# Optimization experiments

Hardware: AMD Instinct MI355X
Metric: run time of the kernel (lower is better)

Reference implementation:

```python
import jax, jax.numpy as jnp
import numpy as np
import math

T = 4096        # block_size / sequence length
E = 2048        # embedding_dim
D = 256         # head_dim


def setup_inputs() -> dict:
    key = jax.random.key(0)
    k_x, k_q, k_k, k_v = jax.random.split(key, 4)
    x = jax.random.normal(k_x, (T, E), dtype=jnp.float32)
    # nn.Linear weights are [out_features, in_features]
    s = 1.0 / math.sqrt(E)
    Wq = jax.random.normal(k_q, (D, E), dtype=jnp.float32) * s
    Wk = jax.random.normal(k_k, (D, E), dtype=jnp.float32) * s
    Wv = jax.random.normal(k_v, (D, E), dtype=jnp.float32) * s
    return {"x": x, "Wq": Wq, "Wk": Wk, "Wv": Wv}


def reference(x, Wq, Wk, Wv):
    # Projections: x @ W.T  (torch Linear, no bias)
    Q = x @ Wq.T            # [T, D]
    K = x @ Wk.T            # [T, D]
    V = x @ Wv.T            # [T, D]
    scale = 1.0 / math.sqrt(Q.shape[-1])
    scores = (Q @ K.T) * scale                      # [T, T]
    causal = jnp.tril(jnp.ones((T, T), dtype=bool))
    scores = jnp.where(causal, scores, jnp.float32(-1e10))
    probs = jax.nn.softmax(scores, axis=-1)         # row softmax (torch legacy dim=1 for 2-D)
    return probs @ V                                # [T, D]
```

## Files before the change

### kernel.cpp

```cpp
#include <hip/hip_runtime.h>
#include <hip/hip_bf16.h>

#define T_DIM 4096
#define E_DIM 2048
#define D_DIM 256

typedef __attribute__((ext_vector_type(4))) float f32x4;
typedef __attribute__((ext_vector_type(8))) short s16x8;

__device__ __forceinline__ unsigned short f2bf(float f) {
  unsigned int u = __float_as_uint(f);
  unsigned int r = (u + 0x7FFFu + ((u >> 16) & 1u)) >> 16;
  return (unsigned short)r;
}
__device__ __forceinline__ float bf2f(unsigned short h) {
  return __uint_as_float(((unsigned int)h) << 16);
}

__device__ __forceinline__ f32x4 mfma16(s16x8 a, s16x8 b, f32x4 c) {
  return __builtin_amdgcn_mfma_f32_16x16x32_bf16(a, b, c, 0, 0, 0);
}

__device__ __forceinline__ void gload_lds16(const void* g, void* l) {
  __builtin_amdgcn_global_load_lds((const __attribute__((address_space(1))) void*)g,
                                   (__attribute__((address_space(3))) void*)l, 16, 0, 0);
}

__device__ __forceinline__ int fbase(int t) {
  int g = t / 3, r = t - 3 * g;
  return 3 * g * (g + 1) / 2 + r * (g + 1);
}

__global__ __launch_bounds__(256) void cvt_kernel(const float* __restrict__ src,
                                                  unsigned short* __restrict__ dst, int n) {
  int i = blockIdx.x * blockDim.x + threadIdx.x;
  if (i * 8 + 8 <= n) {
    float4 a = ((const float4*)src)[i * 2];
    float4 b = ((const float4*)src)[i * 2 + 1];
    uint4 o;
    o.x = (unsigned int)f2bf(a.x) | ((unsigned int)f2bf(a.y) << 16);
    o.y = (unsigned int)f2bf(a.z) | ((unsigned int)f2bf(a.w) << 16);
    o.z = (unsigned int)f2bf(b.x) | ((unsigned int)f2bf(b.y) << 16);
    o.w = (unsigned int)f2bf(b.z) | ((unsigned int)f2bf(b.w) << 16);
    ((uint4*)dst)[i] = o;
  }
}

__global__ __launch_bounds__(256, 3) void qkv_gemm(
    const unsigned short* __restrict__ xb, const unsigned short* __restrict__ wb,
    unsigned short* __restrict__ Qg, unsigned short* __restrict__ Kg,
    unsigned short* __restrict__ Vt) {
  __shared__ __align__(16) unsigned short Al[2][128 * 64];
  __shared__ __align__(16) unsigned short Bl[2][64 * 64];
  int tid = threadIdx.x, wid = tid >> 6, lane = tid & 63;
  int lr = lane & 15, lk = lane >> 4;
  int bi_ = (int)blockIdx.x;
  int xcd = bi_ & 7, kk = bi_ >> 3;
  int mb_ = (kk / 12) * 8 + xcd, nb_ = kk % 12;
  int bm0 = mb_ * 128, bn0 = nb_ * 64;
  int wm = (wid >> 1) * 64, wn = (wid & 1) * 32;

  f32x4 acc[4][2];
#pragma unroll
  for (int m = 0; m < 4; ++m)
#pragma unroll
    for (int n = 0; n < 2; ++n) acc[m][n] = (f32x4){0.f, 0.f, 0.f, 0.f};

#define STAGE_QKV(kt, buf)                                                              \
  {                                                                                     \
    int k0 = (kt)*64;                                                                   \
    _Pragma("unroll") for (int i2 = 0; i2 < 4; ++i2) {                                  \
      int ci = (wid * 4 + i2) * 64 + lane;                                              \
      int row = ci >> 3, cc = ci & 7;                                                   \
      gload_lds16(&xb[(size_t)(bm0 + row) * E_DIM + k0 + ((cc ^ (row & 7)) << 3)],      \
                  &Al[buf][(size_t)(wid * 4 + i2) * 512]);                              \
    }                                                                                   \
    _Pragma("unroll") for (int i2 = 0; i2 < 2; ++i2) {                                  \
      int ci = (wid * 2 + i2) * 64 + lane;                                              \
      int row = ci >> 3, cc = ci & 7;                                                   \
      gload_lds16(&wb[(size_t)(bn0 + row) * E_DIM + k0 + ((cc ^ (row & 7)) << 3)],      \
                  &Bl[buf][(size_t)(wid * 2 + i2) * 512]);                              \
    }                                                                                   \
  }

  STAGE_QKV(0, 0);
  for (int kt = 0; kt < 32; ++kt) {
    int cur = kt & 1;
    __syncthreads();
    if (kt + 1 < 32) STAGE_QKV(kt + 1, cur ^ 1);
    s16x8 af[2][4], bfr[2][2];
#pragma unroll
    for (int c = 0; c < 2; ++c) {
#pragma unroll
      for (int m = 0; m < 4; ++m)
        af[c][m] = *(const s16x8*)&Al[cur][(size_t)(wm + m * 16 + lr) * 64 +
                                           (((c * 4 + lk) ^ (lr & 7)) << 3)];
#pragma unroll
      for (int n = 0; n < 2; ++n)
        bfr[c][n] = *(const s16x8*)&Bl[cur][(size_t)(wn + n * 16 + lr) * 64 +
                                            (((c * 4 + lk) ^ (lr & 7)) << 3)];
    }
#pragma unroll
    for (int c = 0; c < 2; ++c)
#pragma unroll
      for (int m = 0; m < 4; ++m)
#pragma unroll
        for (int n = 0; n < 2; ++n) acc[m][n] = mfma16(af[c][m], bfr[c][n], acc[m][n]);
  }

#pragma unroll
  for (int m = 0; m < 4; ++m) {
    int grow = bm0 + wm + m * 16 + lk * 4;
#pragma unroll
    for (int n = 0; n < 2; ++n) {
      int gcol = bn0 + wn + n * 16 + lr;
      unsigned short h[4];
#pragma unroll
      for (int r = 0; r < 4; ++r) h[r] = f2bf(acc[m][n][r]);
      if (gcol < 256) {
#pragma unroll
        for (int r = 0; r < 4; ++r) Qg[(size_t)(grow + r) * D_DIM + gcol] = h[r];
      } else if (gcol < 512) {
#pragma unroll
        for (int r = 0; r < 4; ++r) Kg[(size_t)(grow + r) * D_DIM + gcol - 256] = h[r];
      } else {
        uint2 w;
        w.x = (unsigned int)h[0] | ((unsigned int)h[1] << 16);
        w.y = (unsigned int)h[2] | ((unsigned int)h[3] << 16);
        *(uint2*)&Vt[(size_t)(gcol - 512) * T_DIM + grow] = w;
      }
    }
  }
#undef STAGE_QKV
}

__global__ __launch_bounds__(256, 2) void attn_kernel(
    const unsigned short* __restrict__ Qg, const unsigned short* __restrict__ Kg,
    const unsigned short* __restrict__ Vt, unsigned short* __restrict__ Opart,
    float* __restrict__ mpart, float* __restrict__ lpart) {
  __shared__ __align__(16) unsigned short Kl[2][32 * 256];
  __shared__ __align__(16) unsigned short Vl[2][256 * 32];
  __shared__ __align__(16) unsigned short Pl[4][16 * 40];

  int b = blockIdx.x;
  int t = (int)sqrtf(6.0f * (float)b + 2.25f);
  if (t > 63) t = 63;
  while (t > 0 && fbase(t) > b) --t;
  while (t < 63 && fbase(t + 1) <= b) ++t;
  int s = b - fbase(t);
  int nt = 2 * t + 2 - 6 * s;
  if (nt > 6) nt = 6;

  int tid = threadIdx.x, wid = tid >> 6, lane = tid & 63;
  int lr = lane & 15, lk = lane >> 4;
  int q0 = t * 64 + wid * 16;
  unsigned short* pl = &Pl[wid][0];

  s16x8 qf[8];
#pragma unroll
  for (int c = 0; c < 8; ++c)
    qf[c] = *(const s16x8*)&Qg[(size_t)(q0 + lr) * D_DIM + c * 32 + lk * 8];

  float m_run = -1e30f, l_run = 0.0f;
  f32x4 Oa[16];
#pragma unroll
  for (int d = 0; d < 16; ++d) Oa[d] = (f32x4){0.f, 0.f, 0.f, 0.f};
  const float scale = 0.0625f;

#define STAGE_KV(j, buf)                                                             \
  {                                                                                  \
    int kv_ = (j)*32;                                                                \
    _Pragma("unroll") for (int i2 = 0; i2 < 4; ++i2) {                               \
      int ci = (wid * 4 + i2) * 64 + lane;                                           \
      int row = ci >> 5, cc = ci & 31;                                               \
      gload_lds16(&Kg[(size_t)(kv_ + row) * D_DIM + ((cc ^ (row & 7)) << 3)],        \
                  &Kl[buf][(size_t)(wid * 4 + i2) * 512]);                           \
    }                                                                                \
    _Pragma("unroll") for (int i2 = 0; i2 < 4; ++i2) {                               \
      int ci = (wid * 4 + i2) * 64 + lane;                                           \
      int rr = ci >> 2, cc = ci & 3;                                                 \
      gload_lds16(&Vt[(size_t)rr * T_DIM + kv_ + ((cc ^ ((rr >> 1) & 3)) << 3)],     \
                  &Vl[buf][(size_t)(wid * 4 + i2) * 512]);                           \
    }                                                                                \
  }

  STAGE_KV(6 * s, 0);
  for (int n = 0; n < nt; ++n) {
    int j = 6 * s + n;
    int kv = j * 32;
    int cur = n & 1;
    __syncthreads();
    if (n + 1 < nt) STAGE_KV(j + 1, cur ^ 1);
    const unsigned short* kl = &Kl[cur][0];
    const unsigned short* vl = &Vl[cur][0];

    f32x4 sa[2];
    sa[0] = (f32x4){0.f, 0.f, 0.f, 0.f};
    sa[1] = (f32x4){0.f, 0.f, 0.f, 0.f};
#pragma unroll
    for (int jb = 0; jb < 2; ++jb) {
      int row = jb * 16 + lr;
#pragma unroll
      for (int c = 0; c < 8; ++c) {
        s16x8 kf = *(const s16x8*)&kl[(size_t)row * 256 + (((c * 4 + lk) ^ (lr & 7)) << 3)];
        sa[jb] = mfma16(kf, qf[c], sa[jb]);
      }
    }

    float tmax = -1e30f;
#pragma unroll
    for (int jb = 0; jb < 2; ++jb) {
#pragma unroll
      for (int r = 0; r < 4; ++r) {
        float v = sa[jb][r] * scale;
        int keyg = kv + jb * 16 + lk * 4 + r;
        if (keyg > q0 + lr) v = -1e30f;
        sa[jb][r] = v;
        tmax = fmaxf(tmax, v);
      }
    }
    tmax = fmaxf(tmax, __shfl_xor(tmax, 16));
    tmax = fmaxf(tmax, __shfl_xor(tmax, 32));
    float m_new = fmaxf(fmaxf(m_run, tmax), -1e29f);
    float alpha = __expf(m_run - m_new);
    float psum = 0.f;
#pragma unroll
    for (int jb = 0; jb < 2; ++jb) {
      float p0 = __expf(sa[jb][0] - m_new);
      float p1 = __expf(sa[jb][1] - m_new);
      float p2 = __expf(sa[jb][2] - m_new);
      float p3 = __expf(sa[jb][3] - m_new);
      psum += (p0 + p1) + (p2 + p3);
      uint2 w;
      w.x = (unsigned int)f2bf(p0) | ((unsigned int)f2bf(p1) << 16);
      w.y = (unsigned int)f2bf(p2) | ((unsigned int)f2bf(p3) << 16);
      *(uint2*)&pl[lr * 40 + jb * 16 + lk * 4] = w;
    }
    psum += __shfl_xor(psum, 16);
    psum += __shfl_xor(psum, 32);
    l_run = l_run * alpha + psum;
    m_run = m_new;
    float al[4];
#pragma unroll
    for (int r = 0; r < 4; ++r) al[r] = __shfl(alpha, lk * 4 + r);
#pragma unroll
    for (int d = 0; d < 16; ++d) {
#pragma unroll
      for (int r = 0; r < 4; ++r) Oa[d][r] *= al[r];
    }

    s16x8 pf = *(const s16x8*)&pl[lr * 40 + lk * 8];
    int vsw = (lk ^ ((lr >> 1) & 3)) << 3;
#pragma unroll
    for (int d = 0; d < 16; ++d) {
      s16x8 vf = *(const s16x8*)&vl[(size_t)(d * 16 + lr) * 32 + vsw];
      Oa[d] = mfma16(pf, vf, Oa[d]);
    }
  }

#pragma unroll
  for (int d = 0; d < 16; ++d) {
    unsigned short h[4];
#pragma unroll
    for (int r = 0; r < 4; ++r) h[r] = f2bf(Oa[d][r]);
    uint2 w;
    w.x = (unsigned int)h[0] | ((unsigned int)h[1] << 16);
    w.y = (unsigned int)h[2] | ((unsigned int)h[3] << 16);
    *(uint2*)&Opart[((size_t)b * 256 + d * 16 + lr) * 64 + wid * 16 + lk * 4] = w;
  }
  if (lane < 16) {
    mpart[(size_t)b * 64 + wid * 16 + lr] = m_run;
    lpart[(size_t)b * 64 + wid * 16 + lr] = l_run;
  }
#undef STAGE_KV
}

__global__ __launch_bounds__(256) void merge_kernel(const unsigned short* __restrict__ Opart,
                                                    const float* __restrict__ mpart,
                                                    const float* __restrict__ lpart,
                                                    float* __restrict__ out) {
  __shared__ float trans[64 * 65];
  int blk = blockIdx.x;
  int t = blk >> 2;
  int d0 = (blk & 3) * 64;
  int q0 = t * 64;
  int ql = threadIdx.x & 63;
  int dg = threadIdx.x >> 6;
  int g = t / 3, r3 = t - 3 * g;
  int base = 3 * g * (g + 1) / 2 + r3 * (g + 1);
  int nb = (t + 3) / 3;

  float M = -1e30f, den = 0.f;
  for (int p = 0; p < nb; ++p) {
    float mp = mpart[(size_t)(base + p) * 64 + ql];
    float lp = lpart[(size_t)(base + p) * 64 + ql];
    float Mn = fmaxf(M, mp);
    float sc = __expf(M - Mn);
    den = den * sc + __expf(mp - Mn) * lp;
    M = Mn;
  }
  float inv = 1.0f / den;

  float acc[16];
#pragma unroll
  for (int k = 0; k < 16; ++k) acc[k] = 0.f;
  for (int p = 0; p < nb; ++p) {
    float w = __expf(mpart[(size_t)(base + p) * 64 + ql] - M);
    const unsigned short* oprow = &Opart[((size_t)(base + p) * 256 + d0 + dg) * 64 + ql];
#pragma unroll
    for (int k = 0; k < 16; ++k) acc[k] += w * bf2f(oprow[(size_t)(4 * k) * 64]);
  }
#pragma unroll
  for (int k = 0; k < 16; ++k) trans[(dg + 4 * k) * 65 + ql] = acc[k] * inv;
  __syncthreads();

#pragma unroll
  for (int k = 0; k < 16; ++k) {
    int qq = (threadIdx.x >> 6) + 4 * k;
    int dd = threadIdx.x & 63;
    out[(size_t)(q0 + qq) * 256 + d0 + dd] = trans[dd * 65 + qq];
  }
}

extern "C" void kernel_launch(void* const* d_in, const int* in_sizes, int n_in,
                              void* d_out, int out_size, void* d_ws, size_t ws_size,
                              hipStream_t stream) {
  const float* x  = (const float*)d_in[0];
  const float* Wq = (const float*)d_in[1];
  const float* Wk = (const float*)d_in[2];
  const float* Wv = (const float*)d_in[3];

  char* ws = (char*)d_ws;
  unsigned short* xb = (unsigned short*)(ws);
  unsigned short* wb = (unsigned short*)(ws + 16777216);
  unsigned short* Qg = (unsigned short*)(ws + 19922944);
  unsigned short* Kg = (unsigned short*)(ws + 22020096);
  unsigned short* Vt = (unsigned short*)(ws + 24117248);
  unsigned short* Opart = (unsigned short*)(ws + 26214400);
  float* mpart = (float*)(ws + 49643520);
  float* lpart = (float*)(ws + 49826560);

  cvt_kernel<<<4096, 256, 0, stream>>>(x, xb, T_DIM * E_DIM);
  cvt_kernel<<<256, 256, 0, stream>>>(Wq, wb, D_DIM * E_DIM);
  cvt_kernel<<<256, 256, 0, stream>>>(Wk, wb + (size_t)D_DIM * E_DIM, D_DIM * E_DIM);
  cvt_kernel<<<256, 256, 0, stream>>>(Wv, wb + (size_t)2 * D_DIM * E_DIM, D_DIM * E_DIM);

  qkv_gemm<<<384, 256, 0, stream>>>(xb, wb, Qg, Kg, Vt);

  attn_kernel<<<715, 256, 0, stream>>>(Qg, Kg, Vt, Opart, mpart, lpart);

  merge_kernel<<<256, 256, 0, stream>>>(Opart, mpart, lpart, (float*)d_out);
}
```

Before: 108.4 us.

## Rework attention split into 128-query tiles, fuse conversions, single-pass merge

Merges the four fp32-to-bf16 conversion launches into one kernel. Replaces the qkv_gemm __syncthreads with raw barriers plus explicit vmcnt waits. Restructures attention to 512-thread blocks covering 128 queries, each handling a 128-key chunk as two 64-key tiles, with a new triangular block mapping interleaved across XCDs and causal masking skipped on off-diagonal tiles. The merge kernel now combines partials in a single online-rescaling pass over 128-query, 32-column tiles. The goal is fewer launches, fewer partials and better reuse per block, at the cost of larger LDS use and fewer, longer blocks.

```diff
diff --git a/kernel.cpp b/kernel.cpp
--- a/kernel.cpp
+++ b/kernel.cpp
@@ -26,24 +26,29 @@
                                    (__attribute__((address_space(3))) void*)l, 16, 0, 0);
 }
 
-__device__ __forceinline__ int fbase(int t) {
-  int g = t / 3, r = t - 3 * g;
-  return 3 * g * (g + 1) / 2 + r * (g + 1);
-}
-
-__global__ __launch_bounds__(256) void cvt_kernel(const float* __restrict__ src,
-                                                  unsigned short* __restrict__ dst, int n) {
-  int i = blockIdx.x * blockDim.x + threadIdx.x;
-  if (i * 8 + 8 <= n) {
-    float4 a = ((const float4*)src)[i * 2];
-    float4 b = ((const float4*)src)[i * 2 + 1];
-    uint4 o;
-    o.x = (unsigned int)f2bf(a.x) | ((unsigned int)f2bf(a.y) << 16);
-    o.y = (unsigned int)f2bf(a.z) | ((unsigned int)f2bf(a.w) << 16);
-    o.z = (unsigned int)f2bf(b.x) | ((unsigned int)f2bf(b.y) << 16);
-    o.w = (unsigned int)f2bf(b.z) | ((unsigned int)f2bf(b.w) << 16);
-    ((uint4*)dst)[i] = o;
-  }
+__global__ __launch_bounds__(256) void cvt_all(const float* __restrict__ x,
+                                               const float* __restrict__ wq,
+                                               const float* __restrict__ wk,
+                                               const float* __restrict__ wv,
+                                               unsigned short* __restrict__ xb,
+                                               unsigned short* __restrict__ wb) {
+  int blk = blockIdx.x;
+  const float* src;
+  unsigned short* dst;
+  int rel;
+  if (blk < 4096)      { src = x;  dst = xb;           rel = blk; }
+  else if (blk < 4352) { src = wq; dst = wb;           rel = blk - 4096; }
+  else if (blk < 4608) { src = wk; dst = wb + 524288;  rel = blk - 4352; }
+  else                 { src = wv; dst = wb + 1048576; rel = blk - 4608; }
+  int i = rel * 256 + threadIdx.x;
+  float4 a = ((const float4*)src)[i * 2];
+  float4 b = ((const float4*)src)[i * 2 + 1];
+  uint4 o;
+  o.x = (unsigned int)f2bf(a.x) | ((unsigned int)f2bf(a.y) << 16);
+  o.y = (unsigned int)f2bf(a.z) | ((unsigned int)f2bf(a.w) << 16);
+  o.z = (unsigned int)f2bf(b.x) | ((unsigned int)f2bf(b.y) << 16);
+  o.w = (unsigned int)f2bf(b.z) | ((unsigned int)f2bf(b.w) << 16);
+  ((uint4*)dst)[i] = o;
 }
 
 __global__ __launch_bounds__(256, 3) void qkv_gemm(
@@ -86,8 +91,14 @@
   STAGE_QKV(0, 0);
   for (int kt = 0; kt < 32; ++kt) {
     int cur = kt & 1;
-    __syncthreads();
-    if (kt + 1 < 32) STAGE_QKV(kt + 1, cur ^ 1);
+    __builtin_amdgcn_s_barrier();
+    if (kt + 1 < 32) {
+      STAGE_QKV(kt + 1, cur ^ 1);
+      asm volatile("s_waitcnt vmcnt(6)" ::: "memory");
+    } else {
+      asm volatile("s_waitcnt vmcnt(0)" ::: "memory");
+    }
+    __builtin_amdgcn_s_barrier();
     s16x8 af[2][4], bfr[2][2];
 #pragma unroll
     for (int c = 0; c < 2; ++c) {
@@ -134,87 +145,93 @@
 #undef STAGE_QKV
 }
 
-__global__ __launch_bounds__(256, 2) void attn_kernel(
+__global__ __launch_bounds__(512, 2) void attn_kernel(
     const unsigned short* __restrict__ Qg, const unsigned short* __restrict__ Kg,
     const unsigned short* __restrict__ Vt, unsigned short* __restrict__ Opart,
     float* __restrict__ mpart, float* __restrict__ lpart) {
-  __shared__ __align__(16) unsigned short Kl[2][32 * 256];
-  __shared__ __align__(16) unsigned short Vl[2][256 * 32];
-  __shared__ __align__(16) unsigned short Pl[4][16 * 40];
-
-  int b = blockIdx.x;
-  int t = (int)sqrtf(6.0f * (float)b + 2.25f);
-  if (t > 63) t = 63;
-  while (t > 0 && fbase(t) > b) --t;
-  while (t < 63 && fbase(t + 1) <= b) ++t;
-  int s = b - fbase(t);
-  int nt = 2 * t + 2 - 6 * s;
-  if (nt > 6) nt = 6;
+  __shared__ __align__(16) unsigned short Kl[2][64 * 256];
+  __shared__ __align__(16) unsigned short Vl[2][256 * 64];
+  __shared__ __align__(16) unsigned short Pl[8][16 * 64];
+
+  int bi = (int)blockIdx.x;
+  int j = (bi & 7) * 66 + (bi >> 3);
+  int t = (int)((sqrtf(8.0f * (float)j + 1.0f) - 1.0f) * 0.5f);
+  while (t > 0 && t * (t + 1) / 2 > j) --t;
+  while ((t + 1) * (t + 2) / 2 <= j) ++t;
+  int s = j - t * (t + 1) / 2;
 
   int tid = threadIdx.x, wid = tid >> 6, lane = tid & 63;
   int lr = lane & 15, lk = lane >> 4;
-  int q0 = t * 64 + wid * 16;
+  int q0w = t * 128 + wid * 16;
   unsigned short* pl = &Pl[wid][0];
 
-  s16x8 qf[8];
-#pragma unroll
-  for (int c = 0; c < 8; ++c)
-    qf[c] = *(const s16x8*)&Qg[(size_t)(q0 + lr) * D_DIM + c * 32 + lk * 8];
-
-  float m_run = -1e30f, l_run = 0.0f;
-  f32x4 Oa[16];
-#pragma unroll
-  for (int d = 0; d < 16; ++d) Oa[d] = (f32x4){0.f, 0.f, 0.f, 0.f};
-  const float scale = 0.0625f;
-
-#define STAGE_KV(j, buf)                                                             \
+#define STAGE_KV(jt, buf)                                                            \
   {                                                                                  \
-    int kv_ = (j)*32;                                                                \
+    int kv_ = (jt)*64;                                                               \
     _Pragma("unroll") for (int i2 = 0; i2 < 4; ++i2) {                               \
-      int ci = (wid * 4 + i2) * 64 + lane;                                           \
-      int row = ci >> 5, cc = ci & 31;                                               \
-      gload_lds16(&Kg[(size_t)(kv_ + row) * D_DIM + ((cc ^ (row & 7)) << 3)],        \
+      int idx = (wid * 4 + i2) * 64 + lane;                                          \
+      int row = idx >> 5, g = idx & 31;                                              \
+      gload_lds16(&Kg[(size_t)(kv_ + row) * D_DIM + ((g ^ (row & 7)) << 3)],         \
                   &Kl[buf][(size_t)(wid * 4 + i2) * 512]);                           \
     }                                                                                \
     _Pragma("unroll") for (int i2 = 0; i2 < 4; ++i2) {                               \
-      int ci = (wid * 4 + i2) * 64 + lane;                                           \
-      int rr = ci >> 2, cc = ci & 3;                                                 \
-      gload_lds16(&Vt[(size_t)rr * T_DIM + kv_ + ((cc ^ ((rr >> 1) & 3)) << 3)],     \
+      int idx = (wid * 4 + i2) * 64 + lane;                                          \
+      int d_ = idx >> 3, g = idx & 7;                                                \
+      gload_lds16(&Vt[(size_t)d_ * T_DIM + kv_ + ((g ^ (d_ & 7)) << 3)],             \
                   &Vl[buf][(size_t)(wid * 4 + i2) * 512]);                           \
     }                                                                                \
   }
 
-  STAGE_KV(6 * s, 0);
-  for (int n = 0; n < nt; ++n) {
-    int j = 6 * s + n;
-    int kv = j * 32;
-    int cur = n & 1;
-    __syncthreads();
-    if (n + 1 < nt) STAGE_KV(j + 1, cur ^ 1);
+  STAGE_KV(2 * s, 0);
+
+  s16x8 qf[8];
+#pragma unroll
+  for (int c = 0; c < 8; ++c)
+    qf[c] = *(const s16x8*)&Qg[(size_t)(q0w + lr) * D_DIM + c * 32 + lk * 8];
+
+  float m_run = -1e30f, l_run = 0.f;
+  f32x4 Oa[16];
+#pragma unroll
+  for (int d = 0; d < 16; ++d) Oa[d] = (f32x4){0.f, 0.f, 0.f, 0.f};
+  const float scale = 0.0625f;
+  int sw = lr & 7;
+
+#pragma unroll
+  for (int n = 0; n < 2; ++n) {
+    int jt = 2 * s + n, kv = jt * 64, cur = n;
+    __builtin_amdgcn_s_barrier();
+    if (n == 0) {
+      STAGE_KV(jt + 1, 1);
+      asm volatile("s_waitcnt vmcnt(8)" ::: "memory");
+    } else {
+      asm volatile("s_waitcnt vmcnt(0)" ::: "memory");
+    }
+    __builtin_amdgcn_s_barrier();
     const unsigned short* kl = &Kl[cur][0];
     const unsigned short* vl = &Vl[cur][0];
 
-    f32x4 sa[2];
-    sa[0] = (f32x4){0.f, 0.f, 0.f, 0.f};
-    sa[1] = (f32x4){0.f, 0.f, 0.f, 0.f};
-#pragma unroll
-    for (int jb = 0; jb < 2; ++jb) {
-      int row = jb * 16 + lr;
+    f32x4 sa[4];
+#pragma unroll
+    for (int jb = 0; jb < 4; ++jb) sa[jb] = (f32x4){0.f, 0.f, 0.f, 0.f};
+#pragma unroll
+    for (int jb = 0; jb < 4; ++jb) {
+      int rowbase = (jb * 16 + lr) * 256;
 #pragma unroll
       for (int c = 0; c < 8; ++c) {
-        s16x8 kf = *(const s16x8*)&kl[(size_t)row * 256 + (((c * 4 + lk) ^ (lr & 7)) << 3)];
+        s16x8 kf = *(const s16x8*)&kl[(size_t)rowbase + (((c * 4 + lk) ^ sw) << 3)];
         sa[jb] = mfma16(kf, qf[c], sa[jb]);
       }
     }
 
+    bool needmask = (kv + 63 > q0w);
+    int myq = q0w + lr;
     float tmax = -1e30f;
 #pragma unroll
-    for (int jb = 0; jb < 2; ++jb) {
+    for (int jb = 0; jb < 4; ++jb) {
 #pragma unroll
       for (int r = 0; r < 4; ++r) {
         float v = sa[jb][r] * scale;
-        int keyg = kv + jb * 16 + lk * 4 + r;
-        if (keyg > q0 + lr) v = -1e30f;
+        if (needmask && (kv + jb * 16 + lk * 4 + r) > myq) v = -1e30f;
         sa[jb][r] = v;
         tmax = fmaxf(tmax, v);
       }
@@ -225,7 +242,7 @@
     float alpha = __expf(m_run - m_new);
     float psum = 0.f;
 #pragma unroll
-    for (int jb = 0; jb < 2; ++jb) {
+    for (int jb = 0; jb < 4; ++jb) {
       float p0 = __expf(sa[jb][0] - m_new);
       float p1 = __expf(sa[jb][1] - m_new);
       float p2 = __expf(sa[jb][2] - m_new);
@@ -234,12 +251,13 @@
       uint2 w;
       w.x = (unsigned int)f2bf(p0) | ((unsigned int)f2bf(p1) << 16);
       w.y = (unsigned int)f2bf(p2) | ((unsigned int)f2bf(p3) << 16);
-      *(uint2*)&pl[lr * 40 + jb * 16 + lk * 4] = w;
+      *(uint2*)&pl[(size_t)lr * 64 + (((jb * 2 + (lk >> 1)) ^ sw) << 3) + (lk & 1) * 4] = w;
     }
     psum += __shfl_xor(psum, 16);
     psum += __shfl_xor(psum, 32);
     l_run = l_run * alpha + psum;
     m_run = m_new;
+
     float al[4];
 #pragma unroll
     for (int r = 0; r < 4; ++r) al[r] = __shfl(alpha, lk * 4 + r);
@@ -249,12 +267,18 @@
       for (int r = 0; r < 4; ++r) Oa[d][r] *= al[r];
     }
 
-    s16x8 pf = *(const s16x8*)&pl[lr * 40 + lk * 8];
-    int vsw = (lk ^ ((lr >> 1) & 3)) << 3;
+    s16x8 pf[2];
+#pragma unroll
+    for (int ks = 0; ks < 2; ++ks)
+      pf[ks] = *(const s16x8*)&pl[(size_t)lr * 64 + (((ks * 4 + lk) ^ sw) << 3)];
 #pragma unroll
     for (int d = 0; d < 16; ++d) {
-      s16x8 vf = *(const s16x8*)&vl[(size_t)(d * 16 + lr) * 32 + vsw];
-      Oa[d] = mfma16(pf, vf, Oa[d]);
+#pragma unroll
+      for (int ks = 0; ks < 2; ++ks) {
+        s16x8 vf = *(const s16x8*)&vl[(size_t)(d * 16 + lr) * 64 +
+                                      (((ks * 4 + lk) ^ sw) << 3)];
+        Oa[d] = mfma16(pf[ks], vf, Oa[d]);
+      }
     }
   }
 
@@ -266,11 +290,11 @@
     uint2 w;
     w.x = (unsigned int)h[0] | ((unsigned int)h[1] << 16);
     w.y = (unsigned int)h[2] | ((unsigned int)h[3] << 16);
-    *(uint2*)&Opart[((size_t)b * 256 + d * 16 + lr) * 64 + wid * 16 + lk * 4] = w;
-  }
-  if (lane < 16) {
-    mpart[(size_t)b * 64 + wid * 16 + lr] = m_run;
-    lpart[(size_t)b * 64 + wid * 16 + lr] = l_run;
+    *(uint2*)&Opart[((size_t)j * 256 + d * 16 + lr) * 128 + wid * 16 + lk * 4] = w;
+  }
+  if (lk == 0) {
+    mpart[(size_t)j * 128 + wid * 16 + lr] = m_run;
+    lpart[(size_t)j * 128 + wid * 16 + lr] = l_run;
   }
 #undef STAGE_KV
 }
@@ -279,46 +303,40 @@
                                                     const float* __restrict__ mpart,
                                                     const float* __restrict__ lpart,
                                                     float* __restrict__ out) {
-  __shared__ float trans[64 * 65];
+  __shared__ float trans[128 * 33];
   int blk = blockIdx.x;
-  int t = blk >> 2;
-  int d0 = (blk & 3) * 64;
-  int q0 = t * 64;
-  int ql = threadIdx.x & 63;
-  int dg = threadIdx.x >> 6;
-  int g = t / 3, r3 = t - 3 * g;
-  int base = 3 * g * (g + 1) / 2 + r3 * (g + 1);
-  int nb = (t + 3) / 3;
+  int t = blk >> 3, d0 = (blk & 7) * 32, q0 = t * 128;
+  int ql = threadIdx.x & 127, dg = threadIdx.x >> 7;
+  int base = t * (t + 1) / 2, np = t + 1;
 
   float M = -1e30f, den = 0.f;
-  for (int p = 0; p < nb; ++p) {
-    float mp = mpart[(size_t)(base + p) * 64 + ql];
-    float lp = lpart[(size_t)(base + p) * 64 + ql];
+  float acc[16];
+#pragma unroll
+  for (int k = 0; k < 16; ++k) acc[k] = 0.f;
+
+#pragma unroll 1
+  for (int p = 0; p < np; ++p) {
+    float mp = mpart[(size_t)(base + p) * 128 + ql];
+    float lp = lpart[(size_t)(base + p) * 128 + ql];
     float Mn = fmaxf(M, mp);
     float sc = __expf(M - Mn);
-    den = den * sc + __expf(mp - Mn) * lp;
+    float w = __expf(mp - Mn);
+    den = den * sc + w * lp;
+    const unsigned short* op = &Opart[((size_t)(base + p) * 256 + d0 + dg) * 128 + ql];
+#pragma unroll
+    for (int k = 0; k < 16; ++k) acc[k] = acc[k] * sc + w * bf2f(op[(size_t)(2 * k) * 128]);
     M = Mn;
   }
   float inv = 1.0f / den;
-
-  float acc[16];
-#pragma unroll
-  for (int k = 0; k < 16; ++k) acc[k] = 0.f;
-  for (int p = 0; p < nb; ++p) {
-    float w = __expf(mpart[(size_t)(base + p) * 64 + ql] - M);
-    const unsigned short* oprow = &Opart[((size_t)(base + p) * 256 + d0 + dg) * 64 + ql];
-#pragma unroll
-    for (int k = 0; k < 16; ++k) acc[k] += w * bf2f(oprow[(size_t)(4 * k) * 64]);
-  }
-#pragma unroll
-  for (int k = 0; k < 16; ++k) trans[(dg + 4 * k) * 65 + ql] = acc[k] * inv;
+#pragma unroll
+  for (int k = 0; k < 16; ++k) trans[ql * 33 + dg + 2 * k] = acc[k] * inv;
   __syncthreads();
 
 #pragma unroll
   for (int k = 0; k < 16; ++k) {
-    int qq = (threadIdx.x >> 6) + 4 * k;
-    int dd = threadIdx.x & 63;
-    out[(size_t)(q0 + qq) * 256 + d0 + dd] = trans[dd * 65 + qq];
+    int q = (threadIdx.x >> 5) + 8 * k;
+    int dd = threadIdx.x & 31;
+    out[(size_t)(q0 + q) * 256 + d0 + dd] = trans[q * 33 + dd];
   }
 }
 
@@ -337,17 +355,11 @@
   unsigned short* Kg = (unsigned short*)(ws + 22020096);
   unsigned short* Vt = (unsigned short*)(ws + 24117248);
   unsigned short* Opart = (unsigned short*)(ws + 26214400);
-  float* mpart = (float*)(ws + 49643520);
-  float* lpart = (float*)(ws + 49826560);
-
-  cvt_kernel<<<4096, 256, 0, stream>>>(x, xb, T_DIM * E_DIM);
-  cvt_kernel<<<256, 256, 0, stream>>>(Wq, wb, D_DIM * E_DIM);
-  cvt_kernel<<<256, 256, 0, stream>>>(Wk, wb + (size_t)D_DIM * E_DIM, D_DIM * E_DIM);
-  cvt_kernel<<<256, 256, 0, stream>>>(Wv, wb + (size_t)2 * D_DIM * E_DIM, D_DIM * E_DIM);
-
+  float* mpart = (float*)(ws + 60817408);
+  float* lpart = (float*)(ws + 61087744);
+
+  cvt_all<<<4864, 256, 0, stream>>>(x, Wq, Wk, Wv, xb, wb);
   qkv_gemm<<<384, 256, 0, stream>>>(xb, wb, Qg, Kg, Vt);
-
-  attn_kernel<<<715, 256, 0, stream>>>(Qg, Kg, Vt, Opart, mpart, lpart);
-
+  attn_kernel<<<528, 512, 0, stream>>>(Qg, Kg, Vt, Opart, mpart, lpart);
   merge_kernel<<<256, 256, 0, stream>>>(Opart, mpart, lpart, (float*)d_out);
 }
```

Measured after the change: 97.90 us. -9.7%, faster.
